# Kernel tuning notes

Hardware: AMD Instinct MI355X
Metric: run time of the kernel (lower is better)

The kernel has to match this reference:

```python
import jax, jax.numpy as jnp
import numpy as np
from jax import lax

B, L = 2, 1024
D_MODEL, D_STATE, EXPAND, D_CONV = 1024, 16, 2, 4
D_INNER = EXPAND * D_MODEL            # 2048
DT_RANK = (D_MODEL + 15) // 16        # 64


def setup_inputs() -> dict:
    key = jax.random.key(0)
    ks = jax.random.split(key, 8)
    g = lambda k, shape, s=0.02: jax.random.normal(k, shape, dtype=jnp.float32) * s
    # Mamba-style A init: A = -exp(A_log), A_log = log(1..d_state) per channel
    A_log = jnp.log(jnp.broadcast_to(
        jnp.arange(1, D_STATE + 1, dtype=jnp.float32), (D_INNER, D_STATE)))
    return {
        "x": jax.random.normal(ks[0], (B, L, D_MODEL), dtype=jnp.float32),
        "W_in": g(ks[1], (D_MODEL, 2 * D_INNER)),
        "conv_w": g(ks[2], (D_INNER, D_CONV), 0.1),
        "conv_b": jnp.zeros((D_INNER,), jnp.float32),
        "W_x": g(ks[3], (D_INNER, DT_RANK + 2 * D_STATE)),
        "W_dt": g(ks[4], (DT_RANK, D_INNER)),
        "b_dt": g(ks[5], (D_INNER,), 0.1),
        "A_log": A_log,
        "D_skip": jnp.ones((D_INNER,), jnp.float32),
        "W_out": g(ks[6], (D_INNER, D_MODEL)),
    }


def reference(x, W_in, conv_w, conv_b, W_x, W_dt, b_dt, A_log, D_skip, W_out):
    # in_proj -> (u, z): [B, L, D_INNER] each
    xz = x @ W_in
    u, z = xz[..., :D_INNER], xz[..., D_INNER:]

    # causal depthwise conv1d, kernel D_CONV (small fixed loop over taps)
    up = jnp.pad(u, ((0, 0), (D_CONV - 1, 0), (0, 0)))
    u = sum(up[:, k:k + L, :] * conv_w[:, k] for k in range(D_CONV)) + conv_b
    u = jax.nn.silu(u)

    # input-dependent dt, B, C
    x_dbl = u @ W_x                                    # [B, L, dt_rank + 2N]
    dt = x_dbl[..., :DT_RANK]
    Bm = x_dbl[..., DT_RANK:DT_RANK + D_STATE]         # [B, L, N]
    Cm = x_dbl[..., DT_RANK + D_STATE:]                # [B, L, N]
    delta = jax.nn.softplus(dt @ W_dt + b_dt)          # [B, L, D]

    A = -jnp.exp(A_log)                                # [D, N]
    deltaA = jnp.exp(jnp.einsum('bld,dn->bldn', delta, A))   # [B, L, D, N]
    dBu = (delta * u)[..., None] * Bm[:, :, None, :]          # [B, L, D, N]

    def step(h, inp):
        dA_t, dBu_t, c_t = inp                         # [B,D,N],[B,D,N],[B,N]
        h = dA_t * h + dBu_t
        y_t = jnp.einsum('bdn,bn->bd', h, c_t)
        return h, y_t

    h0 = jnp.zeros((B, D_INNER, D_STATE), x.dtype)
    _, ys = lax.scan(step, h0,
                     (deltaA.transpose(1, 0, 2, 3),
                      dBu.transpose(1, 0, 2, 3),
                      Cm.transpose(1, 0, 2)))
    y = ys.transpose(1, 0, 2) + u * D_skip             # [B, L, D_INNER]
    y = y * jax.nn.silu(z)                             # gated output
    return y @ W_out                                   # [B, L, D_MODEL]
```

## Files before the change

kernel.cpp:

```cpp
#include <hip/hip_runtime.h>


typedef unsigned short u16;
typedef unsigned int   u32;

#define B_SZ 2
#define L_SZ 1024
#define DM   1024
#define DI   2048
#define DS   16
#define DTR  64
#define NXD  96
#define NCHUNK 32
#define CL   32
#define KSPLIT 8
#define KC     256

typedef __bf16 bf16x8 __attribute__((ext_vector_type(8)));
typedef float  f32x4  __attribute__((ext_vector_type(4)));
typedef u16    u16x8  __attribute__((ext_vector_type(8)));

__device__ __forceinline__ u16 f2bf(float f) {
    u32 x = __float_as_uint(f);
    x += 0x7fffu + ((x >> 16) & 1u);
    return (u16)(x >> 16);
}
__device__ __forceinline__ float bf2f(u16 v) {
    return __uint_as_float(((u32)v) << 16);
}

__device__ __forceinline__ void gld_lds16(const u16* g, u16* l) {
    __builtin_amdgcn_global_load_lds(
        (const __attribute__((address_space(1))) u32*)g,
        (__attribute__((address_space(3))) u32*)l, 16, 0, 0);
}

__device__ __forceinline__ void wg_barrier() {
    __asm__ volatile("" ::: "memory");
    __builtin_amdgcn_s_barrier();
    __asm__ volatile("" ::: "memory");
}
#define WAIT_VM12() __builtin_amdgcn_s_waitcnt(0xF7C)
#define WAIT_VM9()  __builtin_amdgcn_s_waitcnt(0xF79)
#define WAIT_VM8()  __builtin_amdgcn_s_waitcnt(0xF78)
#define WAIT_VM6()  __builtin_amdgcn_s_waitcnt(0xF76)
#define WAIT_VM4()  __builtin_amdgcn_s_waitcnt(0xF74)
#define WAIT_VM3()  __builtin_amdgcn_s_waitcnt(0xF73)
#define WAIT_VM0()  __builtin_amdgcn_s_waitcnt(0xF70)
#define WAIT_LGKM0() __builtin_amdgcn_s_waitcnt(0xC07F)

__global__ __launch_bounds__(256) void gemm128p(
    const u16* __restrict__ A, const u16* __restrict__ BT,
    float* __restrict__ Cf, u16* __restrict__ Cb,
    int M, int N, int K, int op)
{
    __shared__ u16 As[4][128 * 32];
    __shared__ u16 Bs[4][128 * 32];

    const int tid  = threadIdx.x;
    const int wave = tid >> 6;
    const int lane = tid & 63;
    const int q    = lane >> 4;
    const int r16  = lane & 15;
    const int wm   = (wave & 1) * 64;
    const int wn   = (wave >> 1) * 64;
    const int m0   = blockIdx.y * 128;
    const int n0   = blockIdx.x * 128;

    const u16* gA0 = A  + (size_t)(m0 + (tid >> 2))      * K + (tid & 3) * 8;
    const u16* gA1 = A  + (size_t)(m0 + 64 + (tid >> 2)) * K + (tid & 3) * 8;
    const u16* gB0 = BT + (size_t)(n0 + (tid >> 2))      * K + (tid & 3) * 8;
    const u16* gB1 = BT + (size_t)(n0 + 64 + (tid >> 2)) * K + (tid & 3) * 8;

    const int niter = K >> 5;
    const int pre = niter < 3 ? niter : 3;
    for (int p = 0; p < pre; ++p) {
        const int k0 = p * 32;
        gld_lds16(gA0 + k0, &As[p][tid * 8]);
        gld_lds16(gA1 + k0, &As[p][2048 + tid * 8]);
        gld_lds16(gB0 + k0, &Bs[p][tid * 8]);
        gld_lds16(gB1 + k0, &Bs[p][2048 + tid * 8]);
    }

    f32x4 acc[4][4];
#pragma unroll
    for (int s = 0; s < 4; ++s)
#pragma unroll
        for (int j = 0; j < 4; ++j) acc[s][j] = (f32x4){0.f, 0.f, 0.f, 0.f};

    for (int it = 0; it < niter; ++it) {
        if (it + 3 < niter) {
            const int k0 = (it + 3) * 32;
            const int bi = (it + 3) & 3;
            gld_lds16(gA0 + k0, &As[bi][tid * 8]);
            gld_lds16(gA1 + k0, &As[bi][2048 + tid * 8]);
            gld_lds16(gB0 + k0, &Bs[bi][tid * 8]);
            gld_lds16(gB1 + k0, &Bs[bi][2048 + tid * 8]);
            WAIT_VM12();
        } else if (it + 2 < niter) {
            WAIT_VM8();
        } else if (it + 1 < niter) {
            WAIT_VM4();
        } else {
            WAIT_VM0();
        }
        wg_barrier();

        const int cur = it & 3;
        bf16x8 af[4], bfr[4];
#pragma unroll
        for (int s = 0; s < 4; ++s)
            af[s] = *(const bf16x8*)(&As[cur][(wm + s * 16 + r16) * 32 + q * 8]);
#pragma unroll
        for (int j = 0; j < 4; ++j)
            bfr[j] = *(const bf16x8*)(&Bs[cur][(wn + j * 16 + r16) * 32 + q * 8]);
#pragma unroll
        for (int s = 0; s < 4; ++s)
#pragma unroll
            for (int j = 0; j < 4; ++j)
                acc[s][j] = __builtin_amdgcn_mfma_f32_16x16x32_bf16(
                    af[s], bfr[j], acc[s][j], 0, 0, 0);

        wg_barrier();
    }

#pragma unroll
    for (int s = 0; s < 4; ++s) {
        const int row0 = m0 + wm + s * 16 + q * 4;
#pragma unroll
        for (int j = 0; j < 4; ++j) {
            const int col = n0 + wn + j * 16 + r16;
            if (op == 2) {
#pragma unroll
                for (int i = 0; i < 4; ++i)
                    Cb[(size_t)(row0 + i) * N + col] = f2bf(acc[s][j][i]);
            } else {
#pragma unroll
                for (int i = 0; i < 4; ++i)
                    Cf[(size_t)(row0 + i) * N + col] = acc[s][j][i];
            }
        }
    }
}

__global__ __launch_bounds__(256) void gemm_out64(
    const u16* __restrict__ A, const u16* __restrict__ BT,
    float* __restrict__ C, int M, int N, int K)
{
    __shared__ u16 As[4][128 * 32];
    __shared__ u16 Bs[4][64 * 32];

    const int tid  = threadIdx.x;
    const int wave = tid >> 6;
    const int lane = tid & 63;
    const int q    = lane >> 4;
    const int r16  = lane & 15;
    const int wm   = (wave & 1) * 64;
    const int wn   = (wave >> 1) * 32;
    const int ib   = blockIdx.x + (blockIdx.y << 4);
    const int tl   = ((ib & 7) << 5) + (ib >> 3);
    const int m0   = (tl >> 4) * 128;
    const int n0   = (tl & 15) * 64;

    const u16* gA0 = A  + (size_t)(m0 + (tid >> 2))      * K + (tid & 3) * 8;
    const u16* gA1 = A  + (size_t)(m0 + 64 + (tid >> 2)) * K + (tid & 3) * 8;
    const u16* gB0 = BT + (size_t)(n0 + (tid >> 2))      * K + (tid & 3) * 8;

    const int niter = K >> 5;
    const int pre = niter < 3 ? niter : 3;
    for (int p = 0; p < pre; ++p) {
        const int k0 = p * 32;
        gld_lds16(gA0 + k0, &As[p][tid * 8]);
        gld_lds16(gA1 + k0, &As[p][2048 + tid * 8]);
        gld_lds16(gB0 + k0, &Bs[p][tid * 8]);
    }

    f32x4 acc[4][2];
#pragma unroll
    for (int s = 0; s < 4; ++s)
#pragma unroll
        for (int j = 0; j < 2; ++j) acc[s][j] = (f32x4){0.f, 0.f, 0.f, 0.f};

    for (int it = 0; it < niter; ++it) {
        if (it + 3 < niter) {
            const int k0 = (it + 3) * 32;
            const int bi = (it + 3) & 3;
            gld_lds16(gA0 + k0, &As[bi][tid * 8]);
            gld_lds16(gA1 + k0, &As[bi][2048 + tid * 8]);
            gld_lds16(gB0 + k0, &Bs[bi][tid * 8]);
            WAIT_VM9();
        } else if (it + 2 < niter) {
            WAIT_VM6();
        } else if (it + 1 < niter) {
            WAIT_VM3();
        } else {
            WAIT_VM0();
        }
        wg_barrier();

        const int cur = it & 3;
        bf16x8 af[4], bfr[2];
#pragma unroll
        for (int s = 0; s < 4; ++s)
            af[s] = *(const bf16x8*)(&As[cur][(wm + s * 16 + r16) * 32 + q * 8]);
#pragma unroll
        for (int j = 0; j < 2; ++j)
            bfr[j] = *(const bf16x8*)(&Bs[cur][(wn + j * 16 + r16) * 32 + q * 8]);
#pragma unroll
        for (int s = 0; s < 4; ++s)
#pragma unroll
            for (int j = 0; j < 2; ++j)
                acc[s][j] = __builtin_amdgcn_mfma_f32_16x16x32_bf16(
                    af[s], bfr[j], acc[s][j], 0, 0, 0);

        wg_barrier();
    }

#pragma unroll
    for (int s = 0; s < 4; ++s) {
        const int row0 = m0 + wm + s * 16 + q * 4;
#pragma unroll
        for (int j = 0; j < 2; ++j) {
            const int col = n0 + wn + j * 16 + r16;
#pragma unroll
            for (int i = 0; i < 4; ++i)
                C[(size_t)(row0 + i) * N + col] = acc[s][j][i];
        }
    }
}

__global__ __launch_bounds__(256) void gemm_skinny_conv(
    const u16* __restrict__ xz, const u16* __restrict__ BT,
    const float* __restrict__ cw, const float* __restrict__ cb,
    u16* __restrict__ ucbf, float* xdbl)
{
    constexpr int LDT = 40;
    constexpr int XLD = 40;
    __shared__ u16 As[128 * LDT];
    __shared__ u16 Bs[64 * LDT];
    __shared__ u16 sxz[131 * XLD];
    __shared__ float cwS[1024];
    __shared__ float cbS[256];

    const int tid  = threadIdx.x;
    const int wave = tid >> 6;
    const int lane = tid & 63;
    const int q    = lane >> 4;
    const int r16  = lane & 15;
    const int m0   = blockIdx.y * 128;
    const int n0   = blockIdx.x * 64;
    const int kcs  = blockIdx.z * KC;
    const int sr   = tid >> 2;
    const int ss   = (tid & 3) * 8;
    constexpr int XROW = 2 * DI;
    const bool halo_ok = (m0 & (L_SZ - 1)) != 0;

    *(f32x4*)(cwS + tid * 4) = *(const f32x4*)(cw + (size_t)kcs * 4 + tid * 4);
    if (tid < 64)
        *(f32x4*)(cbS + tid * 4) = *(const f32x4*)(cb + kcs + tid * 4);

    f32x4 acc[2][4];
#pragma unroll
    for (int s = 0; s < 2; ++s)
#pragma unroll
        for (int j = 0; j < 4; ++j) acc[s][j] = (f32x4){0.f, 0.f, 0.f, 0.f};

    const int bcol  = n0 + sr;
    const int bcolc = bcol < NXD ? bcol : NXD - 1;

    constexpr int NIT = KC / 32;
    uint4 xa0 = *(const uint4*)(xz + (size_t)(m0 + sr)      * XROW + kcs + ss);
    uint4 xa1 = *(const uint4*)(xz + (size_t)(m0 + 64 + sr) * XROW + kcs + ss);
    uint4 bv  = *(const uint4*)(BT + (size_t)bcolc * DI + kcs + ss);
    uint4 hv  = (uint4){0, 0, 0, 0};
    const int hr  = tid >> 2;
    const int hss = (tid & 3) * 8;
    if (tid < 12 && halo_ok)
        hv = *(const uint4*)(xz + (size_t)(m0 - 3 + hr) * XROW + kcs + hss);

    for (int it = 0; it < NIT; ++it) {
        const int k0 = kcs + it * 32;
        wg_barrier();
        *(uint4*)(sxz + (3 + sr) * XLD + ss)  = xa0;
        *(uint4*)(sxz + (67 + sr) * XLD + ss) = xa1;
        if (tid < 12) *(uint4*)(sxz + hr * XLD + hss) = hv;
        WAIT_LGKM0();
        wg_barrier();

        if (it + 1 < NIT) {
            const int kn = k0 + 32;
            xa0 = *(const uint4*)(xz + (size_t)(m0 + sr)      * XROW + kn + ss);
            xa1 = *(const uint4*)(xz + (size_t)(m0 + 64 + sr) * XROW + kn + ss);
            if (tid < 12 && halo_ok)
                hv = *(const uint4*)(xz + (size_t)(m0 - 3 + hr) * XROW + kn + hss);
        }

        f32x4 cwv[8];
#pragma unroll
        for (int i = 0; i < 8; ++i)
            cwv[i] = *(const f32x4*)(cwS + (it * 32 + ss + i) * 4);
        float s0[8], s1[8];
#pragma unroll
        for (int i = 0; i < 8; ++i) { s0[i] = cbS[it * 32 + ss + i]; s1[i] = s0[i]; }
#pragma unroll
        for (int j = 0; j < 4; ++j) {
            u16x8 t0 = *(const u16x8*)(sxz + (sr + j) * XLD + ss);
            u16x8 t1 = *(const u16x8*)(sxz + (64 + sr + j) * XLD + ss);
#pragma unroll
            for (int i = 0; i < 8; ++i) {
                s0[i] = fmaf(bf2f(t0[i]), cwv[i][j], s0[i]);
                s1[i] = fmaf(bf2f(t1[i]), cwv[i][j], s1[i]);
            }
        }
        u32 p0[4], p1[4];
#pragma unroll
        for (int i = 0; i < 4; ++i) {
            float v0a = s0[2*i],   v0b = s0[2*i+1];
            float v1a = s1[2*i],   v1b = s1[2*i+1];
            v0a = v0a / (1.f + __expf(-v0a));  v0b = v0b / (1.f + __expf(-v0b));
            v1a = v1a / (1.f + __expf(-v1a));  v1b = v1b / (1.f + __expf(-v1b));
            p0[i] = (u32)f2bf(v0a) | ((u32)f2bf(v0b) << 16);
            p1[i] = (u32)f2bf(v1a) | ((u32)f2bf(v1b) << 16);
        }
        uint4 ua = (uint4){p0[0], p0[1], p0[2], p0[3]};
        uint4 ub = (uint4){p1[0], p1[1], p1[2], p1[3]};
        *(uint4*)(As + sr * LDT + ss)        = ua;
        *(uint4*)(As + (64 + sr) * LDT + ss) = ub;
        *(uint4*)(Bs + sr * LDT + ss)        = bv;
        if (n0 == 0) {
            *(uint4*)(ucbf + (size_t)(m0 + sr)      * DI + k0 + ss) = ua;
            *(uint4*)(ucbf + (size_t)(m0 + 64 + sr) * DI + k0 + ss) = ub;
        }
        if (it + 1 < NIT)
            bv = *(const uint4*)(BT + (size_t)bcolc * DI + k0 + 32 + ss);
        WAIT_LGKM0();
        wg_barrier();

        bf16x8 af[2], bfr[4];
#pragma unroll
        for (int s = 0; s < 2; ++s)
            af[s] = *(const bf16x8*)(As + (wave * 32 + s * 16 + r16) * LDT + q * 8);
#pragma unroll
        for (int j = 0; j < 4; ++j)
            bfr[j] = *(const bf16x8*)(Bs + (j * 16 + r16) * LDT + q * 8);
#pragma unroll
        for (int s = 0; s < 2; ++s)
#pragma unroll
            for (int j = 0; j < 4; ++j)
                acc[s][j] = __builtin_amdgcn_mfma_f32_16x16x32_bf16(
                    af[s], bfr[j], acc[s][j], 0, 0, 0);
    }

#pragma unroll
    for (int s = 0; s < 2; ++s) {
        const int row0 = m0 + wave * 32 + s * 16 + q * 4;
#pragma unroll
        for (int j = 0; j < 4; ++j) {
            const int col = n0 + j * 16 + r16;
            if (col < NXD) {
#pragma unroll
                for (int i = 0; i < 4; ++i)
                    atomicAdd(&xdbl[(size_t)(row0 + i) * NXD + col], acc[s][j][i]);
            }
        }
    }
}

__global__ __launch_bounds__(256) void delta_valu(
    const float* __restrict__ xdbl, const float* __restrict__ W_dt,
    const float* __restrict__ bias, float* __restrict__ dlt)
{
    __shared__ float sX[16][64];

    const int tid = threadIdx.x;
    const int col = blockIdx.x * 256 + tid;
    const int r0  = blockIdx.y * 16;

    {
        const int r  = tid >> 4;
        const int c4 = (tid & 15) * 4;
        f32x4 v = *(const f32x4*)(xdbl + (size_t)(r0 + r) * NXD + c4);
        *(f32x4*)(&sX[r][c4]) = v;
    }
    __syncthreads();

    float acc[16];
#pragma unroll
    for (int r = 0; r < 16; ++r) acc[r] = 0.f;

    const float bv = bias[col];
#pragma unroll 4
    for (int k = 0; k < DTR; ++k) {
        float w = W_dt[(size_t)k * DI + col];
#pragma unroll
        for (int r = 0; r < 16; ++r)
            acc[r] = fmaf(sX[r][k], w, acc[r]);
    }

#pragma unroll
    for (int r = 0; r < 16; ++r) {
        float v = acc[r] + bv;
        v = (v > 20.f) ? v : log1pf(__expf(v));
        dlt[(size_t)(r0 + r) * DI + col] = v;
    }
}

__device__ __forceinline__ void tr_tile(
    const float* __restrict__ in, u16* __restrict__ out,
    int R, int C, int tr, int tc, int tid, float (*t)[33])
{
    const int tx = tid & 31, ty = tid >> 5;
    const int r0 = tr * 32, c0 = tc * 32;
#pragma unroll
    for (int i = 0; i < 4; ++i) {
        int r = r0 + ty + i * 8, c = c0 + tx;
        if (r < R && c < C) t[ty + i * 8][tx] = in[(size_t)r * C + c];
    }
    __syncthreads();
#pragma unroll
    for (int i = 0; i < 4; ++i) {
        int oR = c0 + ty + i * 8, oC = r0 + tx;
        if (oR < C && oC < R) out[(size_t)oR * R + oC] = f2bf(t[tx][ty + i * 8]);
    }
}

__global__ __launch_bounds__(256) void prep_kernel(
    const float* __restrict__ x,     u16* __restrict__ xbf,
    const float* __restrict__ W_in,  u16* __restrict__ winT,
    const float* __restrict__ W_out, u16* __restrict__ woutT,
    const float* __restrict__ W_x,   u16* __restrict__ wxT,
    float* __restrict__ xdbl)
{
    __shared__ float t[32][33];
    const int id  = blockIdx.x;
    const int tid = threadIdx.x;
    if (id < 4096) {
        tr_tile(W_in, winT, 1024, 4096, id >> 7, id & 127, tid, t);
    } else if (id < 6144) {
        int i2 = id - 4096;
        tr_tile(W_out, woutT, 2048, 1024, i2 >> 5, i2 & 31, tid, t);
    } else if (id < 6336) {
        int i3 = id - 6144;
        tr_tile(W_x, wxT, 2048, 96, i3 / 3, i3 % 3, tid, t);
    } else if (id < 14528) {
        int i = (id - 6336) * 256 + tid;
        xbf[i] = f2bf(x[i]);
    } else {
        f32x4 z = (f32x4){0.f, 0.f, 0.f, 0.f};
        ((f32x4*)xdbl)[(size_t)(id - 14528) * 256 + tid] = z;
    }
}

#define EXP_TREE(e, p1)                                               \
    {                                                                 \
        float p2 = (p1) * (p1), p4 = p2 * p2, p8 = p4 * p4;           \
        e[0] = (p1);      e[1] = p2;          e[2] = p2 * (p1);       \
        e[3] = p4;        e[4] = p4 * (p1);   e[5] = p4 * p2;         \
        e[6] = p4 * e[2]; e[7] = p8;          e[8] = p8 * (p1);       \
        e[9] = p8 * p2;   e[10] = p8 * e[2];  e[11] = p8 * p4;        \
        e[12] = p8 * e[4]; e[13] = p8 * e[5]; e[14] = p8 * e[6];      \
        e[15] = p8 * p8;                                              \
    }

__global__ __launch_bounds__(512) void scan_fused(
    const float* __restrict__ delta, const u16* __restrict__ ucbf,
    const float* __restrict__ xdbl, const float* __restrict__ A_log,
    const u16* __restrict__ xzbf, const float* __restrict__ Dskip,
    u16* __restrict__ ybf)
{
    __shared__ float sH[16 * 512];
    __shared__ float sSum[512];

    const int tid = threadIdx.x;
    const int b   = blockIdx.y;
    const int d0  = blockIdx.x * 16;
    const int c   = tid >> 4;
    const int dd  = tid & 15;
    const int d   = d0 + dd;

    float Av[16], h[16];
#pragma unroll
    for (int n = 0; n < 16; ++n) {
        Av[n] = -__expf(A_log[d * 16 + n]);
        h[n] = 0.f;
    }

    bool chain = true;
#pragma unroll
    for (int n = 1; n < 16; ++n)
        chain = chain &&
            (fabsf(Av[n] - (float)(n + 1) * Av[0]) <= 1e-5f * fabsf(Av[n]));

    const int rowbase = b * L_SZ + c * CL;
    float sdlt = 0.f;
    if (chain) {
        for (int i = 0; i < CL; ++i) {
            const int row = rowbase + i;
            float dlt = delta[(size_t)row * DI + d];
            float uu  = bf2f(ucbf[(size_t)row * DI + d]);
            float du  = dlt * uu;
            sdlt += dlt;
            const float* xr = xdbl + (size_t)row * NXD;
            float e[16];
            float p1 = __expf(dlt * Av[0]);
            EXP_TREE(e, p1);
#pragma unroll
            for (int n = 0; n < 16; ++n)
                h[n] = fmaf(e[n], h[n], du * xr[DTR + n]);
        }
    } else {
        for (int i = 0; i < CL; ++i) {
            const int row = rowbase + i;
            float dlt = delta[(size_t)row * DI + d];
            float uu  = bf2f(ucbf[(size_t)row * DI + d]);
            float du  = dlt * uu;
            sdlt += dlt;
            const float* xr = xdbl + (size_t)row * NXD;
#pragma unroll
            for (int n = 0; n < 16; ++n) {
                float e = __expf(dlt * Av[n]);
                h[n] = fmaf(e, h[n], du * xr[DTR + n]);
            }
        }
    }
#pragma unroll
    for (int n = 0; n < 16; ++n)
        sH[n * 512 + tid] = h[n];
    sSum[tid] = sdlt;
    __syncthreads();

    if (tid < 256) {
        const int n2  = tid >> 4;
        const int dd2 = tid & 15;
        const float Avn = Av[n2];
        float h0 = 0.f;
        for (int cc = 0; cc < NCHUNK; ++cc) {
            const int o = n2 * 512 + cc * 16 + dd2;
            float hl = sH[o];
            float Pl = __expf(Avn * sSum[cc * 16 + dd2]);
            sH[o] = h0;
            h0 = fmaf(Pl, h0, hl);
        }
    }
    __syncthreads();

#pragma unroll
    for (int n = 0; n < 16; ++n) h[n] = sH[n * 512 + tid];
    const float Dk = Dskip[d];
    if (chain) {
        for (int i = 0; i < CL; ++i) {
            const int row = rowbase + i;
            float dlt = delta[(size_t)row * DI + d];
            float uu  = bf2f(ucbf[(size_t)row * DI + d]);
            float du  = dlt * uu;
            const float* xr = xdbl + (size_t)row * NXD;
            float e[16];
            float p1 = __expf(dlt * Av[0]);
            EXP_TREE(e, p1);
            float y = 0.f;
#pragma unroll
            for (int n = 0; n < 16; ++n) {
                h[n] = fmaf(e[n], h[n], du * xr[DTR + n]);
                y = fmaf(h[n], xr[DTR + DS + n], y);
            }
            float zz = bf2f(xzbf[(size_t)row * (2 * DI) + DI + d]);
            float yv = fmaf(uu, Dk, y) * (zz / (1.f + __expf(-zz)));
            ybf[(size_t)row * DI + d] = f2bf(yv);
        }
    } else {
        for (int i = 0; i < CL; ++i) {
            const int row = rowbase + i;
            float dlt = delta[(size_t)row * DI + d];
            float uu  = bf2f(ucbf[(size_t)row * DI + d]);
            float du  = dlt * uu;
            const float* xr = xdbl + (size_t)row * NXD;
            float y = 0.f;
#pragma unroll
            for (int n = 0; n < 16; ++n) {
                float e = __expf(dlt * Av[n]);
                h[n] = fmaf(e, h[n], du * xr[DTR + n]);
                y = fmaf(h[n], xr[DTR + DS + n], y);
            }
            float zz = bf2f(xzbf[(size_t)row * (2 * DI) + DI + d]);
            float yv = fmaf(uu, Dk, y) * (zz / (1.f + __expf(-zz)));
            ybf[(size_t)row * DI + d] = f2bf(yv);
        }
    }
}

constexpr size_t OFF_DELTA   = 0;
constexpr size_t OFF_XDBL    = OFF_DELTA + 4194304;
constexpr size_t OFF_HBUF    = OFF_XDBL  + 196608;
constexpr size_t OFF_PBUF    = OFF_HBUF  + 2097152;
constexpr size_t OFF_F32_END = OFF_PBUF  + 2097152;
constexpr size_t SOFF_XBF   = 0;
constexpr size_t SOFF_WINT  = SOFF_XBF   + 2097152;
constexpr size_t SOFF_XZBF  = SOFF_WINT  + 4194304;
constexpr size_t SOFF_UCBF  = SOFF_XZBF  + 8388608;
constexpr size_t SOFF_WXT   = SOFF_UCBF  + 4194304;
constexpr size_t SOFF_WDTT  = SOFF_WXT   + 196608;
constexpr size_t SOFF_WOUTT = SOFF_WDTT  + 131072;
constexpr size_t SOFF_YBF   = SOFF_WOUTT + 2097152;

extern "C" void kernel_launch(void* const* d_in, const int* in_sizes, int n_in,
                              void* d_out, int out_size, void* d_ws, size_t ws_size,
                              hipStream_t stream)
{
    const float* x     = (const float*)d_in[0];
    const float* W_in  = (const float*)d_in[1];
    const float* cw    = (const float*)d_in[2];
    const float* cb    = (const float*)d_in[3];
    const float* W_x   = (const float*)d_in[4];
    const float* W_dt  = (const float*)d_in[5];
    const float* b_dt  = (const float*)d_in[6];
    const float* A_log = (const float*)d_in[7];
    const float* Dsk   = (const float*)d_in[8];
    const float* W_out = (const float*)d_in[9];
    float* out = (float*)d_out;

    float* wsf   = (float*)d_ws;
    float* dlt   = wsf + OFF_DELTA;
    float* xdbl  = wsf + OFF_XDBL;
    u16* sb    = (u16*)(wsf + OFF_F32_END);
    u16* xbf   = sb + SOFF_XBF;
    u16* winT  = sb + SOFF_WINT;
    u16* xzbf  = sb + SOFF_XZBF;
    u16* ucbf  = sb + SOFF_UCBF;
    u16* wxT   = sb + SOFF_WXT;
    u16* woutT = sb + SOFF_WOUTT;
    u16* ybf   = sb + SOFF_YBF;

    prep_kernel<<<14720, 256, 0, stream>>>(x, xbf, W_in, winT, W_out, woutT,
                                           W_x, wxT, xdbl);

    gemm128p<<<dim3(32, 16), 256, 0, stream>>>(
        xbf, winT, nullptr, xzbf, 2048, 4096, 1024, 2);

    gemm_skinny_conv<<<dim3(2, 16, KSPLIT), 256, 0, stream>>>(
        xzbf, wxT, cw, cb, ucbf, xdbl);

    delta_valu<<<dim3(DI / 256, DI / 16), 256, 0, stream>>>(
        xdbl, W_dt, b_dt, dlt);

    scan_fused<<<dim3(DI / 16, B_SZ), 512, 0, stream>>>(
        dlt, ucbf, xdbl, A_log, xzbf, Dsk, ybf);

    gemm_out64<<<dim3(16, 16), 256, 0, stream>>>(ybf, woutT, out, 2048, 1024, 2048);
}
```

Baseline: 232.9 us.

## Fuse delta projection and softplus into scan kernel, drop delta_valu launch

Removes the separate delta_valu kernel. Each scan thread now holds its column of W_dt in registers, computes delta on the fly from xdbl during the first scan pass, and caches it in shared memory (64 KB) for the second pass. This cuts one launch and the fp32 delta round-trip through global memory. The cost is 64 extra VGPRs per thread, much more LDS per block (which can lower occupancy) and 64 FMAs per row inside the serial scan. Separately, gemm_out64 drops its swizzled tile mapping for a plain blockIdx mapping.

```diff
diff --git a/kernel.cpp b/kernel.cpp
--- a/kernel.cpp
+++ b/kernel.cpp
@@ -157,10 +157,8 @@
     const int r16  = lane & 15;
     const int wm   = (wave & 1) * 64;
     const int wn   = (wave >> 1) * 32;
-    const int ib   = blockIdx.x + (blockIdx.y << 4);
-    const int tl   = ((ib & 7) << 5) + (ib >> 3);
-    const int m0   = (tl >> 4) * 128;
-    const int n0   = (tl & 15) * 64;
+    const int m0   = blockIdx.y * 128;
+    const int n0   = blockIdx.x * 64;
 
     const u16* gA0 = A  + (size_t)(m0 + (tid >> 2))      * K + (tid & 3) * 8;
     const u16* gA1 = A  + (size_t)(m0 + 64 + (tid >> 2)) * K + (tid & 3) * 8;
@@ -363,45 +361,6 @@
                     atomicAdd(&xdbl[(size_t)(row0 + i) * NXD + col], acc[s][j][i]);
             }
         }
-    }
-}
-
-__global__ __launch_bounds__(256) void delta_valu(
-    const float* __restrict__ xdbl, const float* __restrict__ W_dt,
-    const float* __restrict__ bias, float* __restrict__ dlt)
-{
-    __shared__ float sX[16][64];
-
-    const int tid = threadIdx.x;
-    const int col = blockIdx.x * 256 + tid;
-    const int r0  = blockIdx.y * 16;
-
-    {
-        const int r  = tid >> 4;
-        const int c4 = (tid & 15) * 4;
-        f32x4 v = *(const f32x4*)(xdbl + (size_t)(r0 + r) * NXD + c4);
-        *(f32x4*)(&sX[r][c4]) = v;
-    }
-    __syncthreads();
-
-    float acc[16];
-#pragma unroll
-    for (int r = 0; r < 16; ++r) acc[r] = 0.f;
-
-    const float bv = bias[col];
-#pragma unroll 4
-    for (int k = 0; k < DTR; ++k) {
-        float w = W_dt[(size_t)k * DI + col];
-#pragma unroll
-        for (int r = 0; r < 16; ++r)
-            acc[r] = fmaf(sX[r][k], w, acc[r]);
-    }
-
-#pragma unroll
-    for (int r = 0; r < 16; ++r) {
-        float v = acc[r] + bv;
-        v = (v > 20.f) ? v : log1pf(__expf(v));
-        dlt[(size_t)(r0 + r) * DI + col] = v;
     }
 }
 
@@ -463,12 +422,13 @@
     }
 
 __global__ __launch_bounds__(512) void scan_fused(
-    const float* __restrict__ delta, const u16* __restrict__ ucbf,
-    const float* __restrict__ xdbl, const float* __restrict__ A_log,
-    const u16* __restrict__ xzbf, const float* __restrict__ Dskip,
-    u16* __restrict__ ybf)
+    const u16* __restrict__ ucbf, const float* __restrict__ xdbl,
+    const float* __restrict__ A_log, const u16* __restrict__ xzbf,
+    const float* __restrict__ Dskip, const float* __restrict__ W_dt,
+    const float* __restrict__ b_dt, u16* __restrict__ ybf)
 {
     __shared__ float sH[16 * 512];
+    __shared__ float sDlt[CL * 512];
     __shared__ float sSum[512];
 
     const int tid = threadIdx.x;
@@ -478,6 +438,16 @@
     const int dd  = tid & 15;
     const int d   = d0 + dd;
 
+    f32x4 wv[16];
+#pragma unroll
+    for (int j = 0; j < 16; ++j) {
+        wv[j][0] = W_dt[(size_t)(4 * j + 0) * DI + d];
+        wv[j][1] = W_dt[(size_t)(4 * j + 1) * DI + d];
+        wv[j][2] = W_dt[(size_t)(4 * j + 2) * DI + d];
+        wv[j][3] = W_dt[(size_t)(4 * j + 3) * DI + d];
+    }
+    const float bias = b_dt[d];
+
     float Av[16], h[16];
 #pragma unroll
     for (int n = 0; n < 16; ++n) {
@@ -496,11 +466,21 @@
     if (chain) {
         for (int i = 0; i < CL; ++i) {
             const int row = rowbase + i;
-            float dlt = delta[(size_t)row * DI + d];
+            const float* xr = xdbl + (size_t)row * NXD;
+            float acc = 0.f;
+#pragma unroll
+            for (int j = 0; j < 16; ++j) {
+                f32x4 xq = *(const f32x4*)(xr + 4 * j);
+#pragma unroll
+                for (int l = 0; l < 4; ++l)
+                    acc = fmaf(xq[l], wv[j][l], acc);
+            }
+            float v = acc + bias;
+            float dlt = (v > 20.f) ? v : log1pf(__expf(v));
+            sDlt[i * 512 + tid] = dlt;
+            sdlt += dlt;
             float uu  = bf2f(ucbf[(size_t)row * DI + d]);
             float du  = dlt * uu;
-            sdlt += dlt;
-            const float* xr = xdbl + (size_t)row * NXD;
             float e[16];
             float p1 = __expf(dlt * Av[0]);
             EXP_TREE(e, p1);
@@ -511,11 +491,21 @@
     } else {
         for (int i = 0; i < CL; ++i) {
             const int row = rowbase + i;
-            float dlt = delta[(size_t)row * DI + d];
+            const float* xr = xdbl + (size_t)row * NXD;
+            float acc = 0.f;
+#pragma unroll
+            for (int j = 0; j < 16; ++j) {
+                f32x4 xq = *(const f32x4*)(xr + 4 * j);
+#pragma unroll
+                for (int l = 0; l < 4; ++l)
+                    acc = fmaf(xq[l], wv[j][l], acc);
+            }
+            float v = acc + bias;
+            float dlt = (v > 20.f) ? v : log1pf(__expf(v));
+            sDlt[i * 512 + tid] = dlt;
+            sdlt += dlt;
             float uu  = bf2f(ucbf[(size_t)row * DI + d]);
             float du  = dlt * uu;
-            sdlt += dlt;
-            const float* xr = xdbl + (size_t)row * NXD;
 #pragma unroll
             for (int n = 0; n < 16; ++n) {
                 float e = __expf(dlt * Av[n]);
@@ -550,7 +540,7 @@
     if (chain) {
         for (int i = 0; i < CL; ++i) {
             const int row = rowbase + i;
-            float dlt = delta[(size_t)row * DI + d];
+            float dlt = sDlt[i * 512 + tid];
             float uu  = bf2f(ucbf[(size_t)row * DI + d]);
             float du  = dlt * uu;
             const float* xr = xdbl + (size_t)row * NXD;
@@ -570,7 +560,7 @@
     } else {
         for (int i = 0; i < CL; ++i) {
             const int row = rowbase + i;
-            float dlt = delta[(size_t)row * DI + d];
+            float dlt = sDlt[i * 512 + tid];
             float uu  = bf2f(ucbf[(size_t)row * DI + d]);
             float du  = dlt * uu;
             const float* xr = xdbl + (size_t)row * NXD;
@@ -619,7 +609,6 @@
     float* out = (float*)d_out;
 
     float* wsf   = (float*)d_ws;
-    float* dlt   = wsf + OFF_DELTA;
     float* xdbl  = wsf + OFF_XDBL;
     u16* sb    = (u16*)(wsf + OFF_F32_END);
     u16* xbf   = sb + SOFF_XBF;
@@ -639,11 +628,8 @@
     gemm_skinny_conv<<<dim3(2, 16, KSPLIT), 256, 0, stream>>>(
         xzbf, wxT, cw, cb, ucbf, xdbl);
 
-    delta_valu<<<dim3(DI / 256, DI / 16), 256, 0, stream>>>(
-        xdbl, W_dt, b_dt, dlt);
-
     scan_fused<<<dim3(DI / 16, B_SZ), 512, 0, stream>>>(
-        dlt, ucbf, xdbl, A_log, xzbf, Dsk, ybf);
+        ucbf, xdbl, A_log, xzbf, Dsk, W_dt, b_dt, ybf);
 
     gemm_out64<<<dim3(16, 16), 256, 0, stream>>>(ybf, woutT, out, 2048, 1024, 2048);
 }
```

After: 234.6 us. Within noise of the previous version (+0.7%).
